# Kernel tuning notes

Hardware: AMD Instinct MI355X
Metric: run time of the kernel (lower is better)

The kernel has to match this reference:

```python
import jax, jax.numpy as jnp
import numpy as np

EPS = 1e-6  # all_reduce_params.eps for RESIDUAL_RMS_NORM fusion

TP_SIZE = 8
NUM_TOKENS = 2048
HIDDEN = 8192


def setup_inputs() -> dict:
    key = jax.random.key(0)
    k1, k2, k3 = jax.random.split(key, 3)
    # One shard of the TP-sharded activation per rank: [tp_size, num_tokens, hidden]
    inp = jax.random.normal(k1, (TP_SIZE, NUM_TOKENS, HIDDEN), dtype=jnp.float32)
    residual = jax.random.normal(k2, (NUM_TOKENS, HIDDEN), dtype=jnp.float32)
    norm_weight = jax.random.uniform(k3, (HIDDEN,), dtype=jnp.float32)
    return {"input": inp, "residual": residual, "norm_weight": norm_weight}


def reference(input, residual, norm_weight):
    # MNNVL allreduce (sum across the TP group) -- modeled as sum over rank axis.
    allreduced = jnp.sum(input, axis=0)  # [num_tokens, hidden]
    # Fused RESIDUAL_RMS_NORM: residual_out = allreduce + residual;
    # output = rmsnorm(residual_out) * norm_weight
    residual_out = allreduced + residual
    ms = jnp.mean(jnp.square(residual_out), axis=-1, keepdims=True)
    output = residual_out * jax.lax.rsqrt(ms + EPS) * norm_weight
    return output, residual_out
```

## Files before the change

### kernel.cpp

```cpp
#include <hip/hip_runtime.h>

constexpr int TP     = 8;
constexpr int HIDDEN = 8192;
constexpr int BLOCK  = 256;
constexpr int VPT    = HIDDEN / (BLOCK * 4);
constexpr float EPS  = 1e-6f;

typedef float f32x4 __attribute__((ext_vector_type(4)));

__global__ __launch_bounds__(BLOCK) void ar_residual_rmsnorm_kernel(
    const float* __restrict__ in,
    const float* __restrict__ resid,
    const float* __restrict__ w,
    float* __restrict__ out,
    float* __restrict__ resid_out,
    int ntok)
{
    const int row = blockIdx.x;
    const int tid = threadIdx.x;
    const size_t row_off     = (size_t)row * HIDDEN;
    const size_t rank_stride = (size_t)ntok * HIDDEN;

    f32x4 v[VPT];
    float ss = 0.f;
    #pragma unroll
    for (int p = 0; p < VPT; ++p) {
        const int col = (tid + p * BLOCK) * 4;
        const float* base = in + row_off + col;
        f32x4 x0 = __builtin_nontemporal_load((const f32x4*)(base + 0 * rank_stride));
        f32x4 x1 = __builtin_nontemporal_load((const f32x4*)(base + 1 * rank_stride));
        f32x4 x2 = __builtin_nontemporal_load((const f32x4*)(base + 2 * rank_stride));
        f32x4 x3 = __builtin_nontemporal_load((const f32x4*)(base + 3 * rank_stride));
        f32x4 x4 = __builtin_nontemporal_load((const f32x4*)(base + 4 * rank_stride));
        f32x4 x5 = __builtin_nontemporal_load((const f32x4*)(base + 5 * rank_stride));
        f32x4 x6 = __builtin_nontemporal_load((const f32x4*)(base + 6 * rank_stride));
        f32x4 x7 = __builtin_nontemporal_load((const f32x4*)(base + 7 * rank_stride));
        f32x4 rv = __builtin_nontemporal_load((const f32x4*)(resid + row_off + col));
        f32x4 s01 = x0 + x1, s23 = x2 + x3, s45 = x4 + x5, s67 = x6 + x7;
        f32x4 acc = (s01 + s23) + (s45 + s67) + rv;
        v[p] = acc;
        __builtin_nontemporal_store(acc, (f32x4*)(resid_out + row_off + col));
        ss += acc.x * acc.x + acc.y * acc.y + acc.z * acc.z + acc.w * acc.w;
    }

    #pragma unroll
    for (int o = 32; o > 0; o >>= 1) ss += __shfl_down(ss, o, 64);
    __shared__ float s_ss[BLOCK / 64];
    const int wid = tid >> 6;
    if ((tid & 63) == 0) s_ss[wid] = ss;
    __syncthreads();
    float tot = 0.f;
    #pragma unroll
    for (int i = 0; i < BLOCK / 64; ++i) tot += s_ss[i];

    const float inv = rsqrtf(tot * (1.0f / HIDDEN) + EPS);

    #pragma unroll
    for (int p = 0; p < VPT; ++p) {
        const int col = (tid + p * BLOCK) * 4;
        f32x4 wv = *(const f32x4*)(w + col);
        f32x4 o4 = v[p] * inv * wv;
        __builtin_nontemporal_store(o4, (f32x4*)(out + row_off + col));
    }
}

extern "C" void kernel_launch(void* const* d_in, const int* in_sizes, int n_in,
                              void* d_out, int out_size, void* d_ws, size_t ws_size,
                              hipStream_t stream) {
    const float* in    = (const float*)d_in[0];
    const float* resid = (const float*)d_in[1];
    const float* w     = (const float*)d_in[2];

    const int hidden = in_sizes[2];
    const int ntok   = in_sizes[1] / hidden;

    float* out       = (float*)d_out;
    float* resid_out = (float*)d_out + (size_t)ntok * hidden;

    ar_residual_rmsnorm_kernel<<<ntok, BLOCK, 0, stream>>>(
        in, resid, w, out, resid_out, ntok);
}
```

Baseline: 128.7 us.

## Map one row per wavefront and drop block-level shared reduction

Each 64-lane wavefront now processes a whole 8192-wide row, so the grid shrinks to four rows per block. The sum of squares is reduced only within the wavefront using xor shuffles, which removes the shared-memory write and __syncthreads. Squares are accumulated as vectors and summed horizontally once at the end. In exchange each lane keeps 32 f32x4 values (128 floats) live, and the loops are only partially unrolled, so v[] may be spilled to scratch or cut occupancy in a kernel that is already bandwidth-bound.

```diff
diff --git a/kernel.cpp b/kernel.cpp
--- a/kernel.cpp
+++ b/kernel.cpp
@@ -3,7 +3,7 @@
 constexpr int TP     = 8;
 constexpr int HIDDEN = 8192;
 constexpr int BLOCK  = 256;
-constexpr int VPT    = HIDDEN / (BLOCK * 4);
+constexpr int LPT    = HIDDEN / (64 * 4);
 constexpr float EPS  = 1e-6f;
 
 typedef float f32x4 __attribute__((ext_vector_type(4)));
@@ -16,16 +16,18 @@
     float* __restrict__ resid_out,
     int ntok)
 {
-    const int row = blockIdx.x;
-    const int tid = threadIdx.x;
+    const int tid  = threadIdx.x;
+    const int wid  = tid >> 6;
+    const int lane = tid & 63;
+    const int row  = blockIdx.x * (BLOCK / 64) + wid;
     const size_t row_off     = (size_t)row * HIDDEN;
     const size_t rank_stride = (size_t)ntok * HIDDEN;
 
-    f32x4 v[VPT];
-    float ss = 0.f;
-    #pragma unroll
-    for (int p = 0; p < VPT; ++p) {
-        const int col = (tid + p * BLOCK) * 4;
+    f32x4 v[LPT];
+    f32x4 ssv = {0.f, 0.f, 0.f, 0.f};
+    #pragma unroll 4
+    for (int p = 0; p < LPT; ++p) {
+        const int col = (lane + p * 64) * 4;
         const float* base = in + row_off + col;
         f32x4 x0 = __builtin_nontemporal_load((const f32x4*)(base + 0 * rank_stride));
         f32x4 x1 = __builtin_nontemporal_load((const f32x4*)(base + 1 * rank_stride));
@@ -40,24 +42,18 @@
         f32x4 acc = (s01 + s23) + (s45 + s67) + rv;
         v[p] = acc;
         __builtin_nontemporal_store(acc, (f32x4*)(resid_out + row_off + col));
-        ss += acc.x * acc.x + acc.y * acc.y + acc.z * acc.z + acc.w * acc.w;
+        ssv += acc * acc;
     }
+    float ss = ssv.x + ssv.y + ssv.z + ssv.w;
 
     #pragma unroll
-    for (int o = 32; o > 0; o >>= 1) ss += __shfl_down(ss, o, 64);
-    __shared__ float s_ss[BLOCK / 64];
-    const int wid = tid >> 6;
-    if ((tid & 63) == 0) s_ss[wid] = ss;
-    __syncthreads();
-    float tot = 0.f;
-    #pragma unroll
-    for (int i = 0; i < BLOCK / 64; ++i) tot += s_ss[i];
+    for (int o = 32; o > 0; o >>= 1) ss += __shfl_xor(ss, o, 64);
 
-    const float inv = rsqrtf(tot * (1.0f / HIDDEN) + EPS);
+    const float inv = rsqrtf(ss * (1.0f / HIDDEN) + EPS);
 
-    #pragma unroll
-    for (int p = 0; p < VPT; ++p) {
-        const int col = (tid + p * BLOCK) * 4;
+    #pragma unroll 4
+    for (int p = 0; p < LPT; ++p) {
+        const int col = (lane + p * 64) * 4;
         f32x4 wv = *(const f32x4*)(w + col);
         f32x4 o4 = v[p] * inv * wv;
         __builtin_nontemporal_store(o4, (f32x4*)(out + row_off + col));
@@ -77,6 +73,7 @@
     float* out       = (float*)d_out;
     float* resid_out = (float*)d_out + (size_t)ntok * hidden;
 
-    ar_residual_rmsnorm_kernel<<<ntok, BLOCK, 0, stream>>>(
+    const int rows_per_block = BLOCK / 64;
+    ar_residual_rmsnorm_kernel<<<ntok / rows_per_block, BLOCK, 0, stream>>>(
         in, resid, w, out, resid_out, ntok);
 }
```

Measured after the change: 146.8 us. 1.14x slower.
